# Kernel tuning notes

Hardware: AMD Instinct MI355X
Metric: run time of the kernel (lower is better)

Reference implementation:

```python
import jax, jax.numpy as jnp
import numpy as np

V = 10000   # vocab_size
L = 12      # n_layer
H = 12      # n_head
C = 768     # n_embd
TE = 64     # t_embd
WTE = C - TE
BS = 1024   # block_size
B, T = 4, 1024
D = C // H
EPS = 1e-5


def setup_inputs() -> dict:
    key = jax.random.key(0)
    ks = jax.random.split(key, 12)
    s = 0.02
    def n(k, shape, extra=1.0):
        return jax.random.normal(k, shape, jnp.float32) * (s * extra)
    resid_scale = 1.0 / np.sqrt(2 * L)  # c_proj init std scaling from _init_weights loop
    return {
        'idx': jax.random.randint(ks[0], (B, T), 0, V),
        'ts': jax.random.uniform(ks[1], (B, T), jnp.float32) * 100.0,
        'wte': n(ks[2], (V, WTE)),
        'basis_freq': jnp.asarray(1.0 / 10 ** np.linspace(0, 9, TE), jnp.float32),
        'phase': jnp.zeros((TE,), jnp.float32),
        'wpe': n(ks[3], (BS, C)),
        'ln1_w': jnp.ones((L, C), jnp.float32), 'ln1_b': jnp.zeros((L, C), jnp.float32),
        'qkv_w': n(ks[4], (L, 3 * C, C)), 'qkv_b': jnp.zeros((L, 3 * C), jnp.float32),
        'proj_w': n(ks[5], (L, C, C), resid_scale), 'proj_b': jnp.zeros((L, C), jnp.float32),
        'ln2_w': jnp.ones((L, C), jnp.float32), 'ln2_b': jnp.zeros((L, C), jnp.float32),
        'fc_w': n(ks[6], (L, 4 * C, C)), 'fc_b': jnp.zeros((L, 4 * C), jnp.float32),
        'fc2_w': n(ks[7], (L, C, 4 * C), resid_scale), 'fc2_b': jnp.zeros((L, C), jnp.float32),
        'lnf_w': jnp.ones((C,), jnp.float32), 'lnf_b': jnp.zeros((C,), jnp.float32),
        'lm_w': n(ks[8], (V, C)),
        'tp_w': n(ks[9], (1, C)),
    }


def _ln(x, w, b):
    mu = jnp.mean(x, -1, keepdims=True)
    var = jnp.mean((x - mu) ** 2, -1, keepdims=True)
    return (x - mu) * jax.lax.rsqrt(var + EPS) * w + b


def reference(idx, ts, wte, basis_freq, phase, wpe, ln1_w, ln1_b, qkv_w, qkv_b,
              proj_w, proj_b, ln2_w, ln2_b, fc_w, fc_b, fc2_w, fc2_b,
              lnf_w, lnf_b, lm_w, tp_w):
    Bv, Tv = idx.shape
    tok = wte[idx]                                      # [B,T,C-TE]
    tim = jnp.cos(ts[..., None] * basis_freq + phase)   # TimeEncode -> [B,T,TE]
    x = jnp.concatenate([tok, tim], axis=-1) + wpe[:Tv]
    mask = jnp.tril(jnp.ones((Tv, Tv), bool))
    scale = 1.0 / np.sqrt(D)

    def block(x, p):
        l1w, l1b, qw, qb, pw, pb, l2w, l2b, fw, fb, f2w, f2b = p
        h = _ln(x, l1w, l1b)
        qkv = h @ qw.T + qb                              # [B,T,3C]
        q, k, v = jnp.split(qkv, 3, axis=-1)
        def heads(z):
            return z.reshape(Bv, Tv, H, D).transpose(0, 2, 1, 3)  # [B,H,T,D]
        q, k, v = heads(q), heads(k), heads(v)
        att = jnp.einsum('bhtd,bhsd->bhts', q, k) * scale
        att = jnp.where(mask, att, -jnp.inf)             # causal masked_fill
        att = jax.nn.softmax(att, axis=-1)
        y = jnp.einsum('bhts,bhsd->bhtd', att, v)
        y = y.transpose(0, 2, 1, 3).reshape(Bv, Tv, C)
        x = x + (y @ pw.T + pb)
        h2 = _ln(x, l2w, l2b)
        m = jax.nn.gelu(h2 @ fw.T + fb, approximate=False)  # torch nn.GELU default is exact
        x = x + (m @ f2w.T + f2b)
        return x, None

    x, _ = jax.lax.scan(block, x, (ln1_w, ln1_b, qkv_w, qkv_b, proj_w, proj_b,
                                   ln2_w, ln2_b, fc_w, fc_b, fc2_w, fc2_b))
    x = _ln(x, lnf_w, lnf_b)
    logits = x @ lm_w.T          # [B,T,V]
    tpred = x @ tp_w.T           # [B,T,1]
    return logits, tpred
```

## Files before the change

### kernel.cpp

```cpp
#include <hip/hip_runtime.h>
#include <hip/hip_bf16.h>
#include <math.h>

#define Bb   4
#define Tt   1024
#define Cc   768
#define Hh   12
#define Dd   64
#define Ll   12
#define Vv   10000
#define WTEe 704
#define MTOT 4096

#define QSCALE 0.18033688f

typedef __bf16 bf16x8 __attribute__((ext_vector_type(8)));
typedef float  f32x4  __attribute__((ext_vector_type(4)));
typedef unsigned short u16;

typedef const __attribute__((address_space(1))) void* gptr_t;
typedef __attribute__((address_space(3))) void* lptr_t;

__device__ inline void gload16(const void* g, void* l) {
    __builtin_amdgcn_global_load_lds((gptr_t)g, (lptr_t)l, 16, 0, 0);
}

__device__ inline u16 f2bf(float f) {
    unsigned int u = __float_as_uint(f);
    return (u16)((u + 0x7fffu + ((u >> 16) & 1u)) >> 16);
}
__device__ inline float bf2f(u16 u) { return __uint_as_float(((unsigned)u) << 16); }

__device__ inline float gelu_f(float v) {
    float t = v * (0.797884561f + 0.0356774081f * v * v);
    float e = __expf(2.f * t);
    float th = 1.f - 2.f / (e + 1.f);
    return 0.5f * v * (1.f + th);
}

#if __has_builtin(__builtin_amdgcn_exp2f)
__device__ inline float fast_exp2(float x) { return __builtin_amdgcn_exp2f(x); }
#else
__device__ inline float fast_exp2(float x) { return exp2f(x); }
#endif

#define WAITVM(N)  asm volatile("s_waitcnt vmcnt(" #N ")" ::: "memory")
#define WAITLGKM0() asm volatile("s_waitcnt lgkmcnt(0)" ::: "memory")
#define SCHEDB()   __builtin_amdgcn_sched_barrier(0)
#define SBAR()     __builtin_amdgcn_s_barrier()

__global__ __launch_bounds__(256)
void convert_pack(const float* __restrict__ in, u16* __restrict__ out,
                  int nk8, int K, int rowmod, int scaleLim)
{
    int i = blockIdx.x * 256 + threadIdx.x;
    if (i >= nk8) return;
    int row = (i << 3) / K;
    int col = (i << 3) % K;
    float s = 1.f;
    if (rowmod && (row % rowmod) < scaleLim) s = QSCALE;
    float4 v0 = ((const float4*)in)[2 * i];
    float4 v1 = ((const float4*)in)[2 * i + 1];
    uint4 o;
    o.x = (unsigned)f2bf(v0.x * s) | ((unsigned)f2bf(v0.y * s) << 16);
    o.y = (unsigned)f2bf(v0.z * s) | ((unsigned)f2bf(v0.w * s) << 16);
    o.z = (unsigned)f2bf(v1.x * s) | ((unsigned)f2bf(v1.y * s) << 16);
    o.w = (unsigned)f2bf(v1.z * s) | ((unsigned)f2bf(v1.w * s) << 16);
    int tile = row >> 4, kt = col >> 5;
    int l = (row & 15) | (((col >> 3) & 3) << 4);
    size_t off = (((size_t)tile * (K >> 5) + kt) << 9) + l * 8;
    *(uint4*)(out + off) = o;
}

__global__ __launch_bounds__(256)
void scale_qkvb(const float* __restrict__ in, float* __restrict__ out, int n)
{
    int i = blockIdx.x * 256 + threadIdx.x;
    if (i >= n) return;
    int col = i % (3 * Cc);
    out[i] = in[i] * (col < Cc ? QSCALE : 1.f);
}

__global__ __launch_bounds__(256)
void embed_kernel(const int* __restrict__ idx, const float* __restrict__ ts,
                  const float* __restrict__ wte, const float* __restrict__ freq,
                  const float* __restrict__ ph, const float* __restrict__ wpe,
                  float* __restrict__ x)
{
    const int bt  = blockIdx.x;
    const int t   = bt & (Tt - 1);
    const int tok = idx[bt];
    const float tv = ts[bt];
#pragma unroll
    for (int j = 0; j < 3; ++j) {
        int c = threadIdx.x + (j << 8);
        float val;
        if (c < WTEe) val = wte[(size_t)tok * WTEe + c];
        else {
            int e = c - WTEe;
            val = cosf(tv * freq[e] + ph[e]);
        }
        x[(size_t)bt * Cc + c] = val + wpe[(size_t)t * Cc + c];
    }
}

__global__ __launch_bounds__(256)
void ln_kernel(const float* __restrict__ x, const float* __restrict__ wt,
               const float* __restrict__ bs, u16* __restrict__ out)
{
    const int row = blockIdx.x;
    const int tid = threadIdx.x;
    const float* xr = x + (size_t)row * Cc;
    float v0 = xr[tid], v1 = xr[tid + 256], v2 = xr[tid + 512];
    float s = v0 + v1 + v2;
#pragma unroll
    for (int m = 32; m; m >>= 1) s += __shfl_xor(s, m);
    __shared__ float red[4];
    const int wv = tid >> 6;
    if ((tid & 63) == 0) red[wv] = s;
    __syncthreads();
    float mu = (red[0] + red[1] + red[2] + red[3]) * (1.f / 768.f);
    float d0 = v0 - mu, d1 = v1 - mu, d2 = v2 - mu;
    float s2 = d0 * d0 + d1 * d1 + d2 * d2;
#pragma unroll
    for (int m = 32; m; m >>= 1) s2 += __shfl_xor(s2, m);
    __syncthreads();
    if ((tid & 63) == 0) red[wv] = s2;
    __syncthreads();
    float var = (red[0] + red[1] + red[2] + red[3]) * (1.f / 768.f);
    float rs = rsqrtf(var + 1e-5f);
    u16* orow = out + (size_t)row * Cc;
    orow[tid]       = f2bf(d0 * rs * wt[tid]       + bs[tid]);
    orow[tid + 256] = f2bf(d1 * rs * wt[tid + 256] + bs[tid + 256]);
    orow[tid + 512] = f2bf(d2 * rs * wt[tid + 512] + bs[tid + 512]);
}

__global__ __launch_bounds__(256)
void ln_pack16(const float* __restrict__ x, const float* __restrict__ wt,
               const float* __restrict__ bs, u16* __restrict__ out)
{
    __shared__ float mus[16], rss[16];
    const int tid  = threadIdx.x;
    const int lane = tid & 63;
    const int w    = tid >> 6;
    const int tile = blockIdx.x;
    const int r0   = tile << 4;

#pragma unroll
    for (int rr = 0; rr < 4; ++rr) {
        const int row = r0 + w * 4 + rr;
        const float* xr = x + (size_t)row * Cc;
        float s = 0.f, s2 = 0.f;
#pragma unroll
        for (int j = 0; j < 12; ++j) {
            float v = xr[lane + (j << 6)];
            s += v; s2 += v * v;
        }
#pragma unroll
        for (int m = 32; m; m >>= 1) {
            s  += __shfl_xor(s, m);
            s2 += __shfl_xor(s2, m);
        }
        if (lane == 0) {
            float mu = s * (1.f / 768.f);
            float var = s2 * (1.f / 768.f) - mu * mu;
            mus[w * 4 + rr] = mu;
            rss[w * 4 + rr] = rsqrtf(var + 1e-5f);
        }
    }
    __syncthreads();

    u16* ob = out + ((size_t)tile * 24 << 9);
#pragma unroll
    for (int it = 0; it < 6; ++it) {
        int c   = tid + (it << 8);
        int kt  = c >> 6, l = c & 63;
        int row = l & 15, g = l >> 4;
        int col = kt * 32 + g * 8;
        float mu = mus[row], rs = rss[row];
        const float* xp = x + (size_t)(r0 + row) * Cc + col;
        float4 a = *(const float4*)xp;
        float4 bq = *(const float4*)(xp + 4);
        ushort o[8];
        o[0] = f2bf((a.x - mu) * rs * wt[col]     + bs[col]);
        o[1] = f2bf((a.y - mu) * rs * wt[col + 1] + bs[col + 1]);
        o[2] = f2bf((a.z - mu) * rs * wt[col + 2] + bs[col + 2]);
        o[3] = f2bf((a.w - mu) * rs * wt[col + 3] + bs[col + 3]);
        o[4] = f2bf((bq.x - mu) * rs * wt[col + 4] + bs[col + 4]);
        o[5] = f2bf((bq.y - mu) * rs * wt[col + 5] + bs[col + 5]);
        o[6] = f2bf((bq.z - mu) * rs * wt[col + 6] + bs[col + 6]);
        o[7] = f2bf((bq.w - mu) * rs * wt[col + 7] + bs[col + 7]);
        *(uint4*)(ob + ((size_t)kt << 9) + l * 8) = *(uint4*)o;
    }
}

__device__ inline void st_out(float* p, size_t o, float v) { p[o] = v; }
__device__ inline void st_out(u16*   p, size_t o, float v) { p[o] = f2bf(v); }

template<int EPI, int APK, typename OutT>
__global__ __launch_bounds__(256)
void gemm_bf16(const u16* __restrict__ A, const u16* __restrict__ Wp,
               const float* __restrict__ bias, const float* __restrict__ resid,
               OutT* __restrict__ out, u16* __restrict__ vt, int N, int K)
{
    __shared__ uint4 AF[3][8][64];
    __shared__ uint4 BF[3][8][64];
    const int tid  = threadIdx.x;
    const int lane = tid & 63;
    const int w    = tid >> 6;
    const int wr   = w >> 1, wc = w & 1;
    const int lq   = lane & 15, g = lane >> 4;
    const int m0   = blockIdx.x * 128, n0 = blockIdx.y * 128;
    const int KB   = K >> 5;

    const u16 *ap0, *ap1;
    if (APK) {
        ap0 = A + ((((size_t)(m0 >> 4) + 2 * w) * KB) << 9) + lane * 8;
        ap1 = ap0 + ((size_t)KB << 9);
    } else {
        ap0 = A + (size_t)(m0 + (2 * w) * 16 + lq) * K + g * 8;
        ap1 = ap0 + (size_t)16 * K;
    }

    int tn0 = (n0 >> 4) + 2 * w, tn1 = tn0 + 1;
    const int tmax = (N >> 4) - 1;
    tn0 = tn0 < tmax ? tn0 : tmax;
    tn1 = tn1 < tmax ? tn1 : tmax;
    const u16* bq0 = Wp + (((size_t)tn0 * KB) << 9) + lane * 8;
    const u16* bq1 = Wp + (((size_t)tn1 * KB) << 9) + lane * 8;

    f32x4 acc[4][4] = {};
    const int nk = KB;

#define GSTAGE(s, sl) do {                                               \
        if (APK) {                                                       \
            gload16(ap0 + ((size_t)(s) << 9), &AF[sl][2 * w][lane]);     \
            gload16(ap1 + ((size_t)(s) << 9), &AF[sl][2 * w + 1][lane]); \
        } else {                                                         \
            gload16(ap0 + ((s) << 5), &AF[sl][2 * w][lane]);             \
            gload16(ap1 + ((s) << 5), &AF[sl][2 * w + 1][lane]);         \
        }                                                                \
        gload16(bq0 + ((size_t)(s) << 9), &BF[sl][2 * w][lane]);         \
        gload16(bq1 + ((size_t)(s) << 9), &BF[sl][2 * w + 1][lane]); } while (0)

    GSTAGE(0, 0);
    GSTAGE(1, 1);
    WAITVM(4);
    SCHEDB();
    SBAR();
    SCHEDB();

    int sl = 0;
    for (int t = 0; t < nk; ++t) {
        int sl2 = sl + 2; if (sl2 >= 3) sl2 -= 3;
        if (t + 2 < nk) GSTAGE(t + 2, sl2);

        bf16x8 af[4], bfr[4];
#pragma unroll
        for (int mi = 0; mi < 4; ++mi)
            af[mi] = __builtin_bit_cast(bf16x8, AF[sl][wr * 4 + mi][lane]);
#pragma unroll
        for (int ni = 0; ni < 4; ++ni)
            bfr[ni] = __builtin_bit_cast(bf16x8, BF[sl][wc * 4 + ni][lane]);
        __builtin_amdgcn_s_setprio(1);
#pragma unroll
        for (int mi = 0; mi < 4; ++mi)
#pragma unroll
            for (int ni = 0; ni < 4; ++ni)
                acc[mi][ni] = __builtin_amdgcn_mfma_f32_16x16x32_bf16(
                    af[mi], bfr[ni], acc[mi][ni], 0, 0, 0);
        __builtin_amdgcn_s_setprio(0);

        if (t + 2 < nk) { WAITVM(4); }
        else           { WAITVM(0); }
        SCHEDB();
        SBAR();
        SCHEDB();
        sl = (sl + 1 == 3) ? 0 : sl + 1;
    }
#undef GSTAGE

    if (EPI == 3 && n0 >= 1536) {
#pragma unroll
        for (int mi = 0; mi < 4; ++mi)
#pragma unroll
            for (int ni = 0; ni < 4; ++ni) {
                int col = n0 + wc * 64 + ni * 16 + lq;
                int c2  = col - 1536;
                int hh  = c2 >> 6, dd = c2 & 63;
                int row = m0 + wr * 64 + mi * 16 + g * 4;
                int bb  = row >> 10, tr = row & 1023;
                float bv = bias[col];
                ushort4 o;
                o.x = f2bf(acc[mi][ni][0] + bv);
                o.y = f2bf(acc[mi][ni][1] + bv);
                o.z = f2bf(acc[mi][ni][2] + bv);
                o.w = f2bf(acc[mi][ni][3] + bv);
                *(ushort4*)&vt[(((size_t)bb * Hh + hh) * Dd + dd) * Tt + tr] = o;
            }
        return;
    }

#pragma unroll
    for (int mi = 0; mi < 4; ++mi)
#pragma unroll
        for (int ni = 0; ni < 4; ++ni) {
            int col = n0 + wc * 64 + ni * 16 + lq;
            if (col >= N) continue;
            int row = m0 + wr * 64 + mi * 16 + g * 4;
            float bv = bias ? bias[col] : 0.f;
#pragma unroll
            for (int q = 0; q < 4; ++q) {
                float v = acc[mi][ni][q] + bv;
                size_t o = (size_t)(row + q) * N + col;
                if (EPI == 1) v += resid[o];
                if (EPI == 2) v = gelu_f(v);
                st_out(out, o, v);
            }
        }
}

template<int EPI, typename OutT>
__global__ __launch_bounds__(256)
void gemm_n64(const u16* __restrict__ A, const u16* __restrict__ Wp,
              const float* __restrict__ bias, const float* __restrict__ resid,
              OutT* __restrict__ out, int N, int K)
{
    __shared__ uint4 AF[3][4][64];
    __shared__ uint4 BF[3][8][64];
    const int tid  = threadIdx.x;
    const int lane = tid & 63;
    const int w    = tid >> 6;
    const int wr   = w & 1, wc = w >> 1;
    const int lq   = lane & 15, g = lane >> 4;
    const int m0   = blockIdx.x * 64, n0 = blockIdx.y * 128;
    const int KB   = K >> 5;

    const u16* ap  = A + (size_t)(m0 + w * 16 + lq) * K + g * 8;
    int tn0 = (n0 >> 4) + 2 * w, tn1 = tn0 + 1;
    const int tmax = (N >> 4) - 1;
    tn0 = tn0 < tmax ? tn0 : tmax;
    tn1 = tn1 < tmax ? tn1 : tmax;
    const u16* bq0 = Wp + (((size_t)tn0 * KB) << 9) + lane * 8;
    const u16* bq1 = Wp + (((size_t)tn1 * KB) << 9) + lane * 8;

    f32x4 acc[2][4] = {};
    const int nk = KB;

#define GSTAGE(s, sl) do { int kk_ = (s) << 5;                      \
        gload16(ap  + kk_, &AF[sl][w][lane]);                       \
        gload16(bq0 + ((size_t)(s) << 9), &BF[sl][2 * w][lane]);    \
        gload16(bq1 + ((size_t)(s) << 9), &BF[sl][2 * w + 1][lane]); } while (0)

    GSTAGE(0, 0);
    GSTAGE(1, 1);
    WAITVM(3);
    SCHEDB();
    SBAR();
    SCHEDB();

    int sl = 0;
    for (int t = 0; t < nk; ++t) {
        int sl2 = sl + 2; if (sl2 >= 3) sl2 -= 3;
        if (t + 2 < nk) GSTAGE(t + 2, sl2);

        bf16x8 af[2], bfr[4];
#pragma unroll
        for (int mi = 0; mi < 2; ++mi)
            af[mi] = __builtin_bit_cast(bf16x8, AF[sl][wr * 2 + mi][lane]);
#pragma unroll
        for (int ni = 0; ni < 4; ++ni)
            bfr[ni] = __builtin_bit_cast(bf16x8, BF[sl][wc * 4 + ni][lane]);
        __builtin_amdgcn_s_setprio(1);
#pragma unroll
        for (int mi = 0; mi < 2; ++mi)
#pragma unroll
            for (int ni = 0; ni < 4; ++ni)
                acc[mi][ni] = __builtin_amdgcn_mfma_f32_16x16x32_bf16(
                    af[mi], bfr[ni], acc[mi][ni], 0, 0, 0);
        __builtin_amdgcn_s_setprio(0);

        if (t + 2 < nk) { WAITVM(3); }
        else           { WAITVM(0); }
        SCHEDB();
        SBAR();
        SCHEDB();
        sl = (sl + 1 == 3) ? 0 : sl + 1;
    }
#undef GSTAGE

#pragma unroll
    for (int mi = 0; mi < 2; ++mi)
#pragma unroll
        for (int ni = 0; ni < 4; ++ni) {
            int col = n0 + wc * 64 + ni * 16 + lq;
            if (col >= N) continue;
            int row = m0 + wr * 32 + mi * 16 + g * 4;
            float bv = bias ? bias[col] : 0.f;
#pragma unroll
            for (int q = 0; q < 4; ++q) {
                float v = acc[mi][ni][q] + bv;
                size_t o = (size_t)(row + q) * N + col;
                if (EPI == 1) v += resid[o];
                if (EPI == 2) v = gelu_f(v);
                st_out(out, o, v);
            }
        }
}

template<int EPI, typename OutT>
__global__ __launch_bounds__(512, 2)
void gemm8p(const u16* __restrict__ Apk, const u16* __restrict__ Wp,
            const float* __restrict__ bias, const float* __restrict__ resid,
            OutT* __restrict__ out, int N, int K)
{
    __shared__ uint4 AF[2][16][2][64];
    __shared__ uint4 BF[2][16][2][64];
    const int tid  = threadIdx.x;
    const int lane = tid & 63;
    const int w    = tid >> 6;
    const int wr   = w >> 2, wc = w & 3;
    const int lq   = lane & 15, g = lane >> 4;
    const int m0   = blockIdx.x * 256, n0 = blockIdx.y * 256;
    const int KB   = K >> 5;

    const u16* aq0 = Apk + ((((size_t)(m0 >> 4) + 2 * w) * KB) << 9) + lane * 8;
    const u16* aq1 = aq0 + ((size_t)KB << 9);

    int tn0 = (n0 >> 4) + 2 * w, tn1 = tn0 + 1;
    const int tmax = (N >> 4) - 1;
    tn0 = tn0 < tmax ? tn0 : tmax;
    tn1 = tn1 < tmax ? tn1 : tmax;
    const u16* bq0 = Wp + (((size_t)tn0 * KB) << 9) + lane * 8;
    const u16* bq1 = Wp + (((size_t)tn1 * KB) << 9) + lane * 8;

    f32x4 acc[8][4] = {};
    const int nt = K >> 6;

    gload16(aq0,       &AF[0][2 * w][0][lane]);
    gload16(aq1,       &AF[0][2 * w + 1][0][lane]);
    gload16(bq0,       &BF[0][2 * w][0][lane]);
    gload16(bq1,       &BF[0][2 * w + 1][0][lane]);
    gload16(aq0 + 512, &AF[0][2 * w][1][lane]);
    gload16(aq1 + 512, &AF[0][2 * w + 1][1][lane]);
    gload16(bq0 + 512, &BF[0][2 * w][1][lane]);
    gload16(bq1 + 512, &BF[0][2 * w + 1][1][lane]);
    WAITVM(0);
    SCHEDB();
    SBAR();

    int buf = 0;
    for (int t = 0; t < nt; ++t) {
        const bool more = (t + 1 < nt);
        const size_t bb0 = (size_t)(2 * (t + 1)) << 9;
        bf16x8 a0[4], a1[4], b0[4];

#pragma unroll
        for (int i = 0; i < 4; ++i)
            a0[i] = __builtin_bit_cast(bf16x8, AF[buf][wr * 8 + i][0][lane]);
#pragma unroll
        for (int i = 0; i < 4; ++i)
            b0[i] = __builtin_bit_cast(bf16x8, BF[buf][wc * 4 + i][0][lane]);
        if (more) {
            gload16(aq0 + bb0, &AF[buf ^ 1][2 * w][0][lane]);
            gload16(aq1 + bb0, &AF[buf ^ 1][2 * w + 1][0][lane]);
        }
        SCHEDB();
        SBAR();
        WAITLGKM0();
        SCHEDB();
        __builtin_amdgcn_s_setprio(1);
#pragma unroll
        for (int mi = 0; mi < 4; ++mi)
#pragma unroll
            for (int ni = 0; ni < 4; ++ni)
                acc[mi][ni] = __builtin_amdgcn_mfma_f32_16x16x32_bf16(
                    a0[mi], b0[ni], acc[mi][ni], 0, 0, 0);
        __builtin_amdgcn_s_setprio(0);
        SBAR();

#pragma unroll
        for (int i = 0; i < 4; ++i)
            a1[i] = __builtin_bit_cast(bf16x8, AF[buf][wr * 8 + 4 + i][0][lane]);
        if (more) {
            gload16(bq0 + bb0, &BF[buf ^ 1][2 * w][0][lane]);
            gload16(bq1 + bb0, &BF[buf ^ 1][2 * w + 1][0][lane]);
        }
        SCHEDB();
        SBAR();
        WAITLGKM0();
        SCHEDB();
        __builtin_amdgcn_s_setprio(1);
#pragma unroll
        for (int mi = 0; mi < 4; ++mi)
#pragma unroll
            for (int ni = 0; ni < 4; ++ni)
                acc[4 + mi][ni] = __builtin_amdgcn_mfma_f32_16x16x32_bf16(
                    a1[mi], b0[ni], acc[4 + mi][ni], 0, 0, 0);
        __builtin_amdgcn_s_setprio(0);
        if (more) { WAITVM(4); } else { WAITVM(0); }
        SCHEDB();
        SBAR();

#pragma unroll
        for (int i = 0; i < 4; ++i)
            a0[i] = __builtin_bit_cast(bf16x8, AF[buf][wr * 8 + i][1][lane]);
#pragma unroll
        for (int i = 0; i < 4; ++i)
            b0[i] = __builtin_bit_cast(bf16x8, BF[buf][wc * 4 + i][1][lane]);
        if (more) {
            gload16(aq0 + bb0 + 512, &AF[buf ^ 1][2 * w][1][lane]);
            gload16(aq1 + bb0 + 512, &AF[buf ^ 1][2 * w + 1][1][lane]);
        }
        SCHEDB();
        SBAR();
        WAITLGKM0();
        SCHEDB();
        __builtin_amdgcn_s_setprio(1);
#pragma unroll
        for (int mi = 0; mi < 4; ++mi)
#pragma unroll
            for (int ni = 0; ni < 4; ++ni)
                acc[mi][ni] = __builtin_amdgcn_mfma_f32_16x16x32_bf16(
                    a0[mi], b0[ni], acc[mi][ni], 0, 0, 0);
        __builtin_amdgcn_s_setprio(0);
        SBAR();

#pragma unroll
        for (int i = 0; i < 4; ++i)
            a1[i] = __builtin_bit_cast(bf16x8, AF[buf][wr * 8 + 4 + i][1][lane]);
        if (more) {
            gload16(bq0 + bb0 + 512, &BF[buf ^ 1][2 * w][1][lane]);
            gload16(bq1 + bb0 + 512, &BF[buf ^ 1][2 * w + 1][1][lane]);
        }
        SCHEDB();
        SBAR();
        WAITLGKM0();
        SCHEDB();
        __builtin_amdgcn_s_setprio(1);
#pragma unroll
        for (int mi = 0; mi < 4; ++mi)
#pragma unroll
            for (int ni = 0; ni < 4; ++ni)
                acc[4 + mi][ni] = __builtin_amdgcn_mfma_f32_16x16x32_bf16(
                    a1[mi], b0[ni], acc[4 + mi][ni], 0, 0, 0);
        __builtin_amdgcn_s_setprio(0);
        if (more) { WAITVM(4); } else { WAITVM(0); }
        SCHEDB();
        SBAR();

        buf ^= 1;
    }

#pragma unroll
    for (int mi = 0; mi < 8; ++mi)
#pragma unroll
        for (int ni = 0; ni < 4; ++ni) {
            int col = n0 + wc * 64 + ni * 16 + lq;
            if (col >= N) continue;
            int row = m0 + wr * 128 + mi * 16 + g * 4;
            float bv = bias ? bias[col] : 0.f;
#pragma unroll
            for (int q = 0; q < 4; ++q) {
                float v = acc[mi][ni][q] + bv;
                size_t o = (size_t)(row + q) * N + col;
                if (EPI == 1) v += resid[o];
                if (EPI == 2) v = gelu_f(v);
                st_out(out, o, v);
            }
        }
}

__global__ __launch_bounds__(512)
void attn_mfma(const u16* __restrict__ qkv, const u16* __restrict__ vt,
               u16* __restrict__ y)
{
    __shared__ uint4 KF[2][4][2][64];
    __shared__ uint4 VF[2][4][2][64];

    const int tid  = threadIdx.x;
    const int lane = tid & 63;
    const int w    = tid >> 6;
    const int lq   = lane & 15, g = lane >> 4;
    const int m    = gridDim.x - 1 - blockIdx.x;
    const int bh   = blockIdx.y;
    const int b    = bh / Hh, h = bh % Hh;
    const int wq0  = m * 128 + w * 16;
    const size_t base = (size_t)b * Tt * (3 * Cc);

    const u16* qrow = qkv + base + (size_t)(wq0 + lq) * (3 * Cc) + h * Dd;
    bf16x8 qf0 = __builtin_bit_cast(bf16x8, *(const uint4*)(qrow + g * 8));
    bf16x8 qf1 = __builtin_bit_cast(bf16x8, *(const uint4*)(qrow + 32 + g * 8));

    f32x4 yac[4] = {};
    float lrun = 0.f;

    const int wm = w & 3;
    const u16* kbase = qkv + base + Cc + h * Dd + (size_t)(wm * 16 + lq) * (3 * Cc) + g * 8;
    const u16* vbase = vt + ((size_t)bh * Dd + wm * 16 + lq) * Tt + g * 8;

#define STAGE(c, bi)  do {                                              \
        if (w < 4) {                                                    \
            const u16* kp = kbase + (size_t)(c) * 64 * (3 * Cc);        \
            gload16(kp,      &KF[bi][wm][0][lane]);                     \
            gload16(kp + 32, &KF[bi][wm][1][lane]);                     \
        } else {                                                        \
            const u16* vp = vbase + (c) * 64;                           \
            gload16(vp,      &VF[bi][wm][0][lane]);                     \
            gload16(vp + 32, &VF[bi][wm][1][lane]);                     \
        }                                                               \
    } while (0)

    const int nch = 2 * m + 2;
    STAGE(0, 0);
    WAITVM(0);
    SCHEDB();
    SBAR();

    const int srcb = lq + ((g & 1) << 5);

    int buf = 0;
    for (int c = 0; c < nch; ++c) {
        if (c + 1 < nch) STAGE(c + 1, buf ^ 1);

        f32x4 sc[4] = {};
        __builtin_amdgcn_s_setprio(1);
#pragma unroll
        for (int nt = 0; nt < 4; ++nt) {
            bf16x8 k0 = __builtin_bit_cast(bf16x8, KF[buf][nt][0][lane]);
            bf16x8 k1 = __builtin_bit_cast(bf16x8, KF[buf][nt][1][lane]);
            sc[nt] = __builtin_amdgcn_mfma_f32_16x16x32_bf16(k0, qf0, sc[nt], 0, 0, 0);
            sc[nt] = __builtin_amdgcn_mfma_f32_16x16x32_bf16(k1, qf1, sc[nt], 0, 0, 0);
        }
        __builtin_amdgcn_s_setprio(0);

        const int s0 = c * 64;
        if (s0 + 63 > wq0) {
            const int qg = wq0 + lq;
#pragma unroll
            for (int nt = 0; nt < 4; ++nt) {
                const int kb = s0 + nt * 16 + (g << 2);
#pragma unroll
                for (int j = 0; j < 4; ++j)
                    if (kb + j > qg) sc[nt][j] = -1e30f;
            }
        }

        float ls = 0.f;
#pragma unroll
        for (int nt = 0; nt < 4; ++nt)
#pragma unroll
            for (int j = 0; j < 4; ++j) {
                float p = fast_exp2(sc[nt][j]);
                sc[nt][j] = p;
                ls += p;
            }
        ls += __shfl_xor(ls, 16);
        ls += __shfl_xor(ls, 32);
        lrun += ls;

        unsigned pk[4][2];
#pragma unroll
        for (int nt = 0; nt < 4; ++nt) {
            unsigned u0 = __float_as_uint(sc[nt][0]);
            unsigned u1 = __float_as_uint(sc[nt][1]);
            unsigned u2 = __float_as_uint(sc[nt][2]);
            unsigned u3 = __float_as_uint(sc[nt][3]);
            pk[nt][0] = (u0 >> 16) | (u1 & 0xffff0000u);
            pk[nt][1] = (u2 >> 16) | (u3 & 0xffff0000u);
        }

        unsigned pa0[4], pa1[4];
#pragma unroll
        for (int m2 = 0; m2 < 4; ++m2) {
            int hsel = m2 & 1;
            int src  = srcb + ((m2 >> 1) << 4);
            unsigned lo0 = __shfl(pk[0][hsel], src);
            unsigned hi0 = __shfl(pk[1][hsel], src);
            unsigned lo1 = __shfl(pk[2][hsel], src);
            unsigned hi1 = __shfl(pk[3][hsel], src);
            pa0[m2] = (g >> 1) ? hi0 : lo0;
            pa1[m2] = (g >> 1) ? hi1 : lo1;
        }
        uint4 A0 = make_uint4(pa0[0], pa0[1], pa0[2], pa0[3]);
        uint4 A1 = make_uint4(pa1[0], pa1[1], pa1[2], pa1[3]);
        bf16x8 pA0 = __builtin_bit_cast(bf16x8, A0);
        bf16x8 pA1 = __builtin_bit_cast(bf16x8, A1);

        __builtin_amdgcn_s_setprio(1);
#pragma unroll
        for (int dt = 0; dt < 4; ++dt) {
            bf16x8 vb0 = __builtin_bit_cast(bf16x8, VF[buf][dt][0][lane]);
            bf16x8 vb1 = __builtin_bit_cast(bf16x8, VF[buf][dt][1][lane]);
            yac[dt] = __builtin_amdgcn_mfma_f32_16x16x32_bf16(pA0, vb0, yac[dt], 0, 0, 0);
            yac[dt] = __builtin_amdgcn_mfma_f32_16x16x32_bf16(pA1, vb1, yac[dt], 0, 0, 0);
        }
        __builtin_amdgcn_s_setprio(0);

        if (c + 1 < nch) { WAITVM(0); }
        SCHEDB();
        SBAR();
        buf ^= 1;
    }
#undef STAGE

    f32x4 rl;
#pragma unroll
    for (int j = 0; j < 4; ++j)
        rl[j] = 1.0f / __shfl(lrun, (g << 2) + j);
#pragma unroll
    for (int dt = 0; dt < 4; ++dt)
#pragma unroll
        for (int j = 0; j < 4; ++j)
            y[(size_t)(b * Tt + wq0 + (g << 2) + j) * Cc + h * Dd + dt * 16 + lq]
                = f2bf(yac[dt][j] * rl[j]);
}

__global__ __launch_bounds__(256)
void tpred_kernel(const u16* __restrict__ hp, const float* __restrict__ tp,
                  float* __restrict__ out)
{
    const int row  = blockIdx.x * 4 + (threadIdx.x >> 6);
    const int lane = threadIdx.x & 63;
    const int tile = row >> 4, r15 = row & 15;
    const u16* tb = hp + ((size_t)tile * 24 << 9);
    float s = 0.f;
#pragma unroll
    for (int j = 0; j < 12; ++j) {
        int col = lane + (j << 6);
        int kt = col >> 5, g = (col >> 3) & 3, e = col & 7;
        s += bf2f(tb[((size_t)kt << 9) + (r15 | (g << 4)) * 8 + e]) * tp[col];
    }
#pragma unroll
    for (int m = 32; m; m >>= 1) s += __shfl_xor(s, m);
    if (lane == 0) out[row] = s;
}

extern "C" void kernel_launch(void* const* d_in, const int* in_sizes, int n_in,
                              void* d_out, int out_size, void* d_ws, size_t ws_size,
                              hipStream_t stream)
{
    const int*   idx  = (const int*)d_in[0];
    const float* ts   = (const float*)d_in[1];
    const float* wte  = (const float*)d_in[2];
    const float* freq = (const float*)d_in[3];
    const float* ph   = (const float*)d_in[4];
    const float* wpe  = (const float*)d_in[5];
    const float* ln1w = (const float*)d_in[6];
    const float* ln1b = (const float*)d_in[7];
    const float* qkvw = (const float*)d_in[8];
    const float* qkvb = (const float*)d_in[9];
    const float* pw   = (const float*)d_in[10];
    const float* pb   = (const float*)d_in[11];
    const float* ln2w = (const float*)d_in[12];
    const float* ln2b = (const float*)d_in[13];
    const float* fcw  = (const float*)d_in[14];
    const float* fcb  = (const float*)d_in[15];
    const float* f2w  = (const float*)d_in[16];
    const float* f2b  = (const float*)d_in[17];
    const float* lnfw = (const float*)d_in[18];
    const float* lnfb = (const float*)d_in[19];
    const float* lmw  = (const float*)d_in[20];
    const float* tpw  = (const float*)d_in[21];
    float* out = (float*)d_out;

    const int n_qkvw = 3 * Cc * Cc, n_pw = Cc * Cc, n_fcw = 4 * Cc * Cc;

    char* p = (char*)d_ws;
    float* x    = (float*)p;               p += (size_t)MTOT * Cc * 4;
    u16*   qkvB = (u16*)p;                 p += (size_t)MTOT * 3 * Cc * 2;
    u16*   VtB  = (u16*)p;                 p += (size_t)Bb * Hh * Dd * Tt * 2;
    u16*   hB   = (u16*)p;                 p += (size_t)MTOT * Cc * 2;
    u16*   yB   = (u16*)p;                 p += (size_t)MTOT * Cc * 2;
    u16*   mbB  = (u16*)p;                 p += (size_t)MTOT * 4 * Cc * 2;
    u16*   lmwB = (u16*)p;                 p += (size_t)Vv * Cc * 2;
    float* sbias= (float*)p;               p += (size_t)Ll * 3 * Cc * 4;
    char* wbase = p;

    size_t need_big = (size_t)(wbase - (char*)d_ws)
                    + ((size_t)Ll * (n_qkvw + n_pw + 2 * n_fcw)) * 2;
    bool big = ws_size >= need_big;

    u16 *wqA, *wpA, *wfA, *wf2A;
    if (big) {
        wqA  = (u16*)wbase;                wbase += (size_t)Ll * n_qkvw * 2;
        wpA  = (u16*)wbase;                wbase += (size_t)Ll * n_pw * 2;
        wfA  = (u16*)wbase;                wbase += (size_t)Ll * n_fcw * 2;
        wf2A = (u16*)wbase;
    } else {
        wqA  = (u16*)wbase;                wbase += (size_t)n_qkvw * 2;
        wpA  = (u16*)wbase;                wbase += (size_t)n_pw * 2;
        wfA  = (u16*)wbase;                wbase += (size_t)n_fcw * 2;
        wf2A = (u16*)wbase;
    }

    auto pack = [&](const float* src, u16* dst, size_t rows, int K,
                    int rowmod, int scaleLim) {
        int nk8 = (int)(rows * K / 8);
        convert_pack<<<(nk8 + 255) / 256, 256, 0, stream>>>(
            src, dst, nk8, K, rowmod, scaleLim);
    };

    pack(lmw, lmwB, Vv, Cc, 0, 0);
    {
        int nb = Ll * 3 * Cc;
        scale_qkvb<<<(nb + 255) / 256, 256, 0, stream>>>(qkvb, sbias, nb);
    }
    if (big) {
        pack(qkvw, wqA,  (size_t)Ll * 3 * Cc, Cc, 3 * Cc, Cc);
        pack(pw,   wpA,  (size_t)Ll * Cc,     Cc, 0, 0);
        pack(fcw,  wfA,  (size_t)Ll * 4 * Cc, Cc, 0, 0);
        pack(f2w,  wf2A, (size_t)Ll * Cc, 4 * Cc, 0, 0);
    }
    embed_kernel<<<MTOT, 256, 0, stream>>>(idx, ts, wte, freq, ph, wpe, x);

    for (int l = 0; l < Ll; ++l) {
        u16 *wqB, *wpB, *wfB, *wf2B;
        if (big) {
            wqB  = wqA  + (size_t)l * n_qkvw;
            wpB  = wpA  + (size_t)l * n_pw;
            wfB  = wfA  + (size_t)l * n_fcw;
            wf2B = wf2A + (size_t)l * n_fcw;
        } else {
            wqB = wqA; wpB = wpA; wfB = wfA; wf2B = wf2A;
            pack(qkvw + (size_t)l * n_qkvw, wqB, 3 * Cc, Cc, 3 * Cc, Cc);
            pack(pw   + (size_t)l * n_pw,   wpB, Cc,     Cc, 0, 0);
            pack(fcw  + (size_t)l * n_fcw,  wfB, 4 * Cc, Cc, 0, 0);
            pack(f2w  + (size_t)l * n_fcw,  wf2B, Cc, 4 * Cc, 0, 0);
        }

        ln_pack16<<<MTOT / 16, 256, 0, stream>>>(x, ln1w + l * Cc, ln1b + l * Cc, hB);
        gemm_bf16<3, 1, u16><<<dim3(32, 18), 256, 0, stream>>>(
            hB, wqB, sbias + (size_t)l * 3 * Cc, nullptr, qkvB, VtB, 3 * Cc, Cc);
        attn_mfma<<<dim3(Tt / 128, Bb * Hh), 512, 0, stream>>>(qkvB, VtB, yB);
        gemm_n64<1, float><<<dim3(64, 6), 256, 0, stream>>>(
            yB, wpB, pb + (size_t)l * Cc, x, x, Cc, Cc);
        ln_pack16<<<MTOT / 16, 256, 0, stream>>>(x, ln2w + l * Cc, ln2b + l * Cc, hB);
        gemm_bf16<2, 1, u16><<<dim3(32, 24), 256, 0, stream>>>(
            hB, wfB, fcb + (size_t)l * 4 * Cc, nullptr, mbB, nullptr, 4 * Cc, Cc);
        gemm_n64<1, float><<<dim3(64, 6), 256, 0, stream>>>(
            mbB, wf2B, f2b + (size_t)l * Cc, x, x, Cc, 4 * Cc);
    }

    ln_pack16<<<MTOT / 16, 256, 0, stream>>>(x, lnfw, lnfb, hB);
    gemm8p<0, float><<<dim3(16, 40), 512, 0, stream>>>(
        hB, lmwB, nullptr, nullptr, out, Vv, Cc);
    tpred_kernel<<<MTOT / 4, 256, 0, stream>>>(hB, tpw, out + (size_t)MTOT * Vv);
}
```

Baseline: 2.698 ms.

## Write K and V from QKV GEMM in MFMA fragment-packed layout for attention

The QKV GEMM epilogue now splits its output into a dense Q buffer, a K buffer packed into 512-element fragment tiles, and a V buffer packed in the transposed fragment order that attention consumes. The attention kernel then stages K and V with fully contiguous 16-byte global-to-LDS loads instead of strided row gathers. The aim is better coalescing and fewer memory transactions in attention. The cost is a K epilogue that does scattered 2-byte stores. The unused ln_kernel is also removed.

Measured after the change: 2.935 ms. 1.09x slower.

```diff
diff --git a/kernel.cpp b/kernel.cpp
--- a/kernel.cpp
+++ b/kernel.cpp
@@ -102,37 +102,6 @@
         }
         x[(size_t)bt * Cc + c] = val + wpe[(size_t)t * Cc + c];
     }
-}
-
-__global__ __launch_bounds__(256)
-void ln_kernel(const float* __restrict__ x, const float* __restrict__ wt,
-               const float* __restrict__ bs, u16* __restrict__ out)
-{
-    const int row = blockIdx.x;
-    const int tid = threadIdx.x;
-    const float* xr = x + (size_t)row * Cc;
-    float v0 = xr[tid], v1 = xr[tid + 256], v2 = xr[tid + 512];
-    float s = v0 + v1 + v2;
-#pragma unroll
-    for (int m = 32; m; m >>= 1) s += __shfl_xor(s, m);
-    __shared__ float red[4];
-    const int wv = tid >> 6;
-    if ((tid & 63) == 0) red[wv] = s;
-    __syncthreads();
-    float mu = (red[0] + red[1] + red[2] + red[3]) * (1.f / 768.f);
-    float d0 = v0 - mu, d1 = v1 - mu, d2 = v2 - mu;
-    float s2 = d0 * d0 + d1 * d1 + d2 * d2;
-#pragma unroll
-    for (int m = 32; m; m >>= 1) s2 += __shfl_xor(s2, m);
-    __syncthreads();
-    if ((tid & 63) == 0) red[wv] = s2;
-    __syncthreads();
-    float var = (red[0] + red[1] + red[2] + red[3]) * (1.f / 768.f);
-    float rs = rsqrtf(var + 1e-5f);
-    u16* orow = out + (size_t)row * Cc;
-    orow[tid]       = f2bf(d0 * rs * wt[tid]       + bs[tid]);
-    orow[tid + 256] = f2bf(d1 * rs * wt[tid + 256] + bs[tid + 256]);
-    orow[tid + 512] = f2bf(d2 * rs * wt[tid + 512] + bs[tid + 512]);
 }
 
 __global__ __launch_bounds__(256)
@@ -201,7 +170,8 @@
 __global__ __launch_bounds__(256)
 void gemm_bf16(const u16* __restrict__ A, const u16* __restrict__ Wp,
                const float* __restrict__ bias, const float* __restrict__ resid,
-               OutT* __restrict__ out, u16* __restrict__ vt, int N, int K)
+               OutT* __restrict__ out, u16* __restrict__ vt, u16* __restrict__ kb,
+               int N, int K)
 {
     __shared__ uint4 AF[3][8][64];
     __shared__ uint4 BF[3][8][64];
@@ -280,24 +250,63 @@
     }
 #undef GSTAGE
 
-    if (EPI == 3 && n0 >= 1536) {
-#pragma unroll
-        for (int mi = 0; mi < 4; ++mi)
-#pragma unroll
-            for (int ni = 0; ni < 4; ++ni) {
-                int col = n0 + wc * 64 + ni * 16 + lq;
-                int c2  = col - 1536;
-                int hh  = c2 >> 6, dd = c2 & 63;
-                int row = m0 + wr * 64 + mi * 16 + g * 4;
-                int bb  = row >> 10, tr = row & 1023;
-                float bv = bias[col];
-                ushort4 o;
-                o.x = f2bf(acc[mi][ni][0] + bv);
-                o.y = f2bf(acc[mi][ni][1] + bv);
-                o.z = f2bf(acc[mi][ni][2] + bv);
-                o.w = f2bf(acc[mi][ni][3] + bv);
-                *(ushort4*)&vt[(((size_t)bb * Hh + hh) * Dd + dd) * Tt + tr] = o;
-            }
+    if (EPI == 3) {
+        if (n0 < Cc) {
+#pragma unroll
+            for (int mi = 0; mi < 4; ++mi)
+#pragma unroll
+                for (int ni = 0; ni < 4; ++ni) {
+                    int col = n0 + wc * 64 + ni * 16 + lq;
+                    int row = m0 + wr * 64 + mi * 16 + g * 4;
+                    float bv = bias[col];
+#pragma unroll
+                    for (int q = 0; q < 4; ++q)
+                        ((u16*)out)[(size_t)(row + q) * Cc + col]
+                            = f2bf(acc[mi][ni][q] + bv);
+                }
+        } else if (n0 < 2 * Cc) {
+#pragma unroll
+            for (int mi = 0; mi < 4; ++mi)
+#pragma unroll
+                for (int ni = 0; ni < 4; ++ni) {
+                    int col = n0 + wc * 64 + ni * 16 + lq;
+                    int c2  = col - Cc, hh = c2 >> 6, dd = c2 & 63;
+                    int slab = dd >> 5, gk = (dd >> 3) & 3, e = dd & 7;
+                    int row = m0 + wr * 64 + mi * 16 + g * 4;
+                    int bh  = (row >> 10) * Hh + hh;
+                    float bv = bias[col];
+#pragma unroll
+                    for (int q = 0; q < 4; ++q) {
+                        int key = (row + q) & 1023;
+                        size_t off = ((((size_t)bh * 64 + (key >> 4)) * 2 + slab) << 9)
+                                   + (size_t)((key & 15) | (gk << 4)) * 8 + e;
+                        kb[off] = f2bf(acc[mi][ni][q] + bv);
+                    }
+                }
+        } else {
+#pragma unroll
+            for (int mi = 0; mi < 4; ++mi)
+#pragma unroll
+                for (int ni = 0; ni < 4; ++ni) {
+                    int col = n0 + wc * 64 + ni * 16 + lq;
+                    int c2  = col - 2 * Cc, hh = c2 >> 6, dd = c2 & 63;
+                    int dt  = dd >> 4;
+                    int row = m0 + wr * 64 + mi * 16 + g * 4;
+                    int bh  = (row >> 10) * Hh + hh;
+                    int key0 = row & 1023;
+                    int lane_v = (dd & 15) | (((key0 >> 3) & 3) << 4);
+                    int vtile  = key0 >> 5;
+                    int e0     = key0 & 7;
+                    float bv = bias[col];
+                    ushort4 o;
+                    o.x = f2bf(acc[mi][ni][0] + bv);
+                    o.y = f2bf(acc[mi][ni][1] + bv);
+                    o.z = f2bf(acc[mi][ni][2] + bv);
+                    o.w = f2bf(acc[mi][ni][3] + bv);
+                    *(ushort4*)&vt[((((size_t)bh * 4 + dt) * 32 + vtile) << 9)
+                                   + lane_v * 8 + e0] = o;
+                }
+        }
         return;
     }
 
@@ -572,8 +581,8 @@
 }
 
 __global__ __launch_bounds__(512)
-void attn_mfma(const u16* __restrict__ qkv, const u16* __restrict__ vt,
-               u16* __restrict__ y)
+void attn_mfma(const u16* __restrict__ qB, const u16* __restrict__ KBp,
+               const u16* __restrict__ VBp, u16* __restrict__ y)
 {
     __shared__ uint4 KF[2][4][2][64];
     __shared__ uint4 VF[2][4][2][64];
@@ -586,9 +595,8 @@
     const int bh   = blockIdx.y;
     const int b    = bh / Hh, h = bh % Hh;
     const int wq0  = m * 128 + w * 16;
-    const size_t base = (size_t)b * Tt * (3 * Cc);
-
-    const u16* qrow = qkv + base + (size_t)(wq0 + lq) * (3 * Cc) + h * Dd;
+
+    const u16* qrow = qB + (size_t)(b * Tt + wq0 + lq) * Cc + h * Dd;
     bf16x8 qf0 = __builtin_bit_cast(bf16x8, *(const uint4*)(qrow + g * 8));
     bf16x8 qf1 = __builtin_bit_cast(bf16x8, *(const uint4*)(qrow + 32 + g * 8));
 
@@ -596,18 +604,18 @@
     float lrun = 0.f;
 
     const int wm = w & 3;
-    const u16* kbase = qkv + base + Cc + h * Dd + (size_t)(wm * 16 + lq) * (3 * Cc) + g * 8;
-    const u16* vbase = vt + ((size_t)bh * Dd + wm * 16 + lq) * Tt + g * 8;
+    const u16* kroot = KBp + (((size_t)bh * 64 + wm) * 2 << 9) + lane * 8;
+    const u16* vroot = VBp + (((size_t)bh * 4 + wm) * 32 << 9) + lane * 8;
 
 #define STAGE(c, bi)  do {                                              \
         if (w < 4) {                                                    \
-            const u16* kp = kbase + (size_t)(c) * 64 * (3 * Cc);        \
-            gload16(kp,      &KF[bi][wm][0][lane]);                     \
-            gload16(kp + 32, &KF[bi][wm][1][lane]);                     \
+            const u16* kp = kroot + (((size_t)(c) * 4 * 2) << 9);       \
+            gload16(kp,       &KF[bi][wm][0][lane]);                    \
+            gload16(kp + 512, &KF[bi][wm][1][lane]);                    \
         } else {                                                        \
-            const u16* vp = vbase + (c) * 64;                           \
-            gload16(vp,      &VF[bi][wm][0][lane]);                     \
-            gload16(vp + 32, &VF[bi][wm][1][lane]);                     \
+            const u16* vp = vroot + (((size_t)(c) * 2) << 9);           \
+            gload16(vp,       &VF[bi][wm][0][lane]);                    \
+            gload16(vp + 512, &VF[bi][wm][1][lane]);                    \
         }                                                               \
     } while (0)
 
@@ -768,8 +776,9 @@
 
     char* p = (char*)d_ws;
     float* x    = (float*)p;               p += (size_t)MTOT * Cc * 4;
-    u16*   qkvB = (u16*)p;                 p += (size_t)MTOT * 3 * Cc * 2;
-    u16*   VtB  = (u16*)p;                 p += (size_t)Bb * Hh * Dd * Tt * 2;
+    u16*   qB   = (u16*)p;                 p += (size_t)MTOT * Cc * 2;
+    u16*   KBp  = (u16*)p;                 p += (size_t)Bb * Hh * 64 * 2 * 512 * 2;
+    u16*   VBp  = (u16*)p;                 p += (size_t)Bb * Hh * 4 * 32 * 512 * 2;
     u16*   hB   = (u16*)p;                 p += (size_t)MTOT * Cc * 2;
     u16*   yB   = (u16*)p;                 p += (size_t)MTOT * Cc * 2;
     u16*   mbB  = (u16*)p;                 p += (size_t)MTOT * 4 * Cc * 2;
@@ -831,13 +840,13 @@
 
         ln_pack16<<<MTOT / 16, 256, 0, stream>>>(x, ln1w + l * Cc, ln1b + l * Cc, hB);
         gemm_bf16<3, 1, u16><<<dim3(32, 18), 256, 0, stream>>>(
-            hB, wqB, sbias + (size_t)l * 3 * Cc, nullptr, qkvB, VtB, 3 * Cc, Cc);
-        attn_mfma<<<dim3(Tt / 128, Bb * Hh), 512, 0, stream>>>(qkvB, VtB, yB);
+            hB, wqB, sbias + (size_t)l * 3 * Cc, nullptr, qB, VBp, KBp, 3 * Cc, Cc);
+        attn_mfma<<<dim3(Tt / 128, Bb * Hh), 512, 0, stream>>>(qB, KBp, VBp, yB);
         gemm_n64<1, float><<<dim3(64, 6), 256, 0, stream>>>(
             yB, wpB, pb + (size_t)l * Cc, x, x, Cc, Cc);
         ln_pack16<<<MTOT / 16, 256, 0, stream>>>(x, ln2w + l * Cc, ln2b + l * Cc, hB);
         gemm_bf16<2, 1, u16><<<dim3(32, 24), 256, 0, stream>>>(
-            hB, wfB, fcb + (size_t)l * 4 * Cc, nullptr, mbB, nullptr, 4 * Cc, Cc);
+            hB, wfB, fcb + (size_t)l * 4 * Cc, nullptr, mbB, nullptr, nullptr, 4 * Cc, Cc);
         gemm_n64<1, float><<<dim3(64, 6), 256, 0, stream>>>(
             mbB, wf2B, f2b + (size_t)l * Cc, x, x, Cc, 4 * Cc);
     }
```
